# Performance work log

Hardware: AMD Instinct MI355X
Metric: run time of the kernel (lower is better)

Reference implementation:

```python
import jax, jax.numpy as jnp
import numpy as np

N_NODES = 50000
N_EDGES = 1600000
NFEAT, NHID, NCLASS = 512, 128, 40


def setup_inputs() -> dict:
    key = jax.random.key(0)
    ks = jax.random.split(key, 10)
    x = jax.random.normal(ks[0], (N_NODES, NFEAT), dtype=jnp.float32)
    edge_src = jax.random.randint(ks[1], (N_EDGES,), 0, N_NODES, dtype=jnp.int32)
    edge_dst = jax.random.randint(ks[2], (N_EDGES,), 0, N_NODES, dtype=jnp.int32)
    edge_weight = jax.random.uniform(ks[3], (N_EDGES,), dtype=jnp.float32)
    # GraphConvolution params: gc1 (nfeat->nhid), one additional (nhid->nhid), gc2 (nhid->nclass)
    s1 = 1.0 / np.sqrt(NHID)
    s2 = 1.0 / np.sqrt(NCLASS)
    W1 = jax.random.uniform(ks[4], (NFEAT, NHID), minval=-s1, maxval=s1, dtype=jnp.float32)
    b1 = jax.random.uniform(ks[5], (NHID,), minval=-s1, maxval=s1, dtype=jnp.float32)
    Wh = jax.random.uniform(ks[6], (NHID, NHID), minval=-s1, maxval=s1, dtype=jnp.float32)
    bh = jax.random.uniform(ks[7], (NHID,), minval=-s1, maxval=s1, dtype=jnp.float32)
    W2 = jax.random.uniform(ks[8], (NHID, NCLASS), minval=-s2, maxval=s2, dtype=jnp.float32)
    b2 = jax.random.uniform(ks[9], (NCLASS,), minval=-s2, maxval=s2, dtype=jnp.float32)
    return {"x": x, "edge_src": edge_src, "edge_dst": edge_dst, "edge_weight": edge_weight,
            "W1": W1, "b1": b1, "Wh": Wh, "bh": bh, "W2": W2, "b2": b2}


def reference(x, edge_src, edge_dst, edge_weight, W1, b1, Wh, bh, W2, b2):
    def spmm(h):
        # out[i] = sum_j adj[i, j] * h[j]  with adj given as weighted edge list (src=j, dst=i)
        return jax.ops.segment_sum(edge_weight[:, None] * h[edge_src], edge_dst,
                                   num_segments=x.shape[0])

    def gconv(h, W, b):
        return spmm(h @ W) + b  # dense transform then sparse aggregation

    h = jax.nn.relu(gconv(x, W1, b1))       # gc1
    h = jax.nn.relu(gconv(h, Wh, bh))        # additional hidden layer
    h = gconv(h, W2, b2)                     # gc2
    return jax.nn.log_softmax(h, axis=1)
```

## Files before the change

kernel.cpp:

```cpp
#include <hip/hip_runtime.h>
#include <hip/hip_bf16.h>
#include <hip/hip_fp8.h>
#include <math.h>

#define N_NODES 50000
#define N_EDGES 1600000
#define NFEAT 512
#define NHID 128
#define NCLASS 40

#define NBUCKETS 196
#define BUCKET_CAP 16384

typedef __attribute__((ext_vector_type(8))) short bf16x8;
typedef __attribute__((ext_vector_type(4))) float f32x4;
typedef __attribute__((ext_vector_type(2))) float f32x2;

static __device__ __forceinline__ float asfloat_u32(unsigned int u) {
    union { unsigned int u; float f; } c;
    c.u = u;
    return c.f;
}
static __device__ __forceinline__ unsigned int asu32_f(float f) {
    union { float f; unsigned int u; } c;
    c.f = f;
    return c.u;
}
static __device__ __forceinline__ unsigned short f2bf(float f) {
    union { float f; unsigned int u; } c;
    c.f = f;
    unsigned int r = c.u + 0x7FFFu + ((c.u >> 16) & 1u);
    return (unsigned short)(r >> 16);
}

static __device__ __forceinline__ float fp8_to_f32_sw(unsigned int x) {
    float m = asfloat_u32((x & 0x7Fu) << 20) * 0x1p+120f;
    return asfloat_u32(asu32_f(m) | ((x & 0x80u) << 24));
}
static __device__ __forceinline__ void dq4(unsigned int u, float* f) {
#if __has_builtin(__builtin_amdgcn_cvt_pk_f32_fp8)
    f32x2 lo = __builtin_amdgcn_cvt_pk_f32_fp8(u, false);
    f32x2 hi = __builtin_amdgcn_cvt_pk_f32_fp8(u, true);
    f[0] = lo[0]; f[1] = lo[1]; f[2] = hi[0]; f[3] = hi[1];
#else
    f[0] = fp8_to_f32_sw(u & 0xFFu);
    f[1] = fp8_to_f32_sw((u >> 8) & 0xFFu);
    f[2] = fp8_to_f32_sw((u >> 16) & 0xFFu);
    f[3] = fp8_to_f32_sw((u >> 24) & 0xFFu);
#endif
}
static __device__ __forceinline__ unsigned char f2fp8(float f) {
#if __has_builtin(__builtin_amdgcn_cvt_pk_fp8_f32)
    int v = __builtin_amdgcn_cvt_pk_fp8_f32(f, f, 0, false);
    return (unsigned char)(v & 0xFF);
#else
    __hip_fp8_e4m3 h(f);
    return (unsigned char)h.__x;
#endif
}

__global__ __launch_bounds__(256) void prep_kernel(const float* __restrict__ W1,
                                                   unsigned short* __restrict__ Wt1,
                                                   const float* __restrict__ Wh,
                                                   unsigned short* __restrict__ Wth,
                                                   const float* __restrict__ W2,
                                                   unsigned short* __restrict__ Wt2,
                                                   int* __restrict__ bucketCursor) {
    int idx = blockIdx.x * 256 + threadIdx.x;
    if (idx < NFEAT * NHID) {
        int k = idx >> 7;
        int n = idx & 127;
        Wt1[(size_t)n * NFEAT + k] = f2bf(W1[idx]);
    } else if (idx < NFEAT * NHID + NHID * NHID) {
        int j = idx - NFEAT * NHID;
        int k = j >> 7;
        int n = j & 127;
        Wth[(size_t)n * NHID + k] = f2bf(Wh[j]);
    } else if (idx < NFEAT * NHID + NHID * NHID + 64 * NHID) {
        int j = idx - (NFEAT * NHID + NHID * NHID);
        int n = j & 63;
        int k = j >> 6;
        Wt2[(size_t)n * NHID + k] = (n < NCLASS) ? f2bf(W2[(size_t)k * NCLASS + n]) : 0;
    } else {
        int j = idx - (NFEAT * NHID + NHID * NHID + 64 * NHID);
        if (j < NBUCKETS) bucketCursor[j] = j * BUCKET_CAP;
    }
}

#define LDPB 72
#define GEMM_LDS_BYTES (128 * LDPB * 2)

template <bool A_IS_BF16, bool OUT_FP8>
static __device__ __forceinline__ void gemm64_body(const void* __restrict__ Ap,
                                                   const unsigned short* __restrict__ Wt,
                                                   void* __restrict__ Cv,
                                                   const int M, const int K,
                                                   char* smem, int bid) {
    unsigned short* Bs = (unsigned short*)smem;
    const int tid = threadIdx.x;
    const int wave = tid >> 6;
    const int lane = tid & 63;
    const int ln = lane & 15;
    const int quad = lane >> 4;
    const int row0 = bid * 64;

    const int arow = row0 + wave * 16 + ln;
    const bool aOk = arow < M;
    const unsigned short* Abf = (const unsigned short*)Ap + (size_t)arow * K + quad * 8;
    const float* Af = (const float*)Ap + (size_t)arow * K + quad * 8;

    const int bn = tid >> 1;
    const int bk = (tid & 1) * 32;
    const unsigned short* Bg = Wt + (size_t)bn * K + bk;

    f32x4 acc[8];
#pragma unroll
    for (int t = 0; t < 8; ++t) acc[t] = (f32x4){0.f, 0.f, 0.f, 0.f};

    for (int kc = 0; kc < K; kc += 64) {
        bf16x8 qb0 = *(const bf16x8*)(Bg + kc);
        bf16x8 qb1 = *(const bf16x8*)(Bg + kc + 8);
        bf16x8 qb2 = *(const bf16x8*)(Bg + kc + 16);
        bf16x8 qb3 = *(const bf16x8*)(Bg + kc + 24);

        bf16x8 a0, a1;
        if (A_IS_BF16) {
            if (aOk) {
                a0 = *(const bf16x8*)(Abf + kc);
                a1 = *(const bf16x8*)(Abf + kc + 32);
            } else {
#pragma unroll
                for (int j = 0; j < 8; ++j) { a0[j] = 0; a1[j] = 0; }
            }
        } else {
            if (aOk) {
                float4 f0 = *(const float4*)(Af + kc);
                float4 f1 = *(const float4*)(Af + kc + 4);
                float4 f2 = *(const float4*)(Af + kc + 32);
                float4 f3 = *(const float4*)(Af + kc + 36);
                a0[0] = (short)f2bf(f0.x); a0[1] = (short)f2bf(f0.y);
                a0[2] = (short)f2bf(f0.z); a0[3] = (short)f2bf(f0.w);
                a0[4] = (short)f2bf(f1.x); a0[5] = (short)f2bf(f1.y);
                a0[6] = (short)f2bf(f1.z); a0[7] = (short)f2bf(f1.w);
                a1[0] = (short)f2bf(f2.x); a1[1] = (short)f2bf(f2.y);
                a1[2] = (short)f2bf(f2.z); a1[3] = (short)f2bf(f2.w);
                a1[4] = (short)f2bf(f3.x); a1[5] = (short)f2bf(f3.y);
                a1[6] = (short)f2bf(f3.z); a1[7] = (short)f2bf(f3.w);
            } else {
#pragma unroll
                for (int j = 0; j < 8; ++j) { a0[j] = 0; a1[j] = 0; }
            }
        }

        __syncthreads();
        *(bf16x8*)&Bs[bn * LDPB + bk] = qb0;
        *(bf16x8*)&Bs[bn * LDPB + bk + 8] = qb1;
        *(bf16x8*)&Bs[bn * LDPB + bk + 16] = qb2;
        *(bf16x8*)&Bs[bn * LDPB + bk + 24] = qb3;
        __syncthreads();

#pragma unroll
        for (int t = 0; t < 8; ++t) {
            bf16x8 b0 = *(const bf16x8*)&Bs[(t * 16 + ln) * LDPB + quad * 8];
            acc[t] = __builtin_amdgcn_mfma_f32_16x16x32_bf16(a0, b0, acc[t], 0, 0, 0);
        }
#pragma unroll
        for (int t = 0; t < 8; ++t) {
            bf16x8 b1 = *(const bf16x8*)&Bs[(t * 16 + ln) * LDPB + 32 + quad * 8];
            acc[t] = __builtin_amdgcn_mfma_f32_16x16x32_bf16(a1, b1, acc[t], 0, 0, 0);
        }
    }

    if (OUT_FP8) {
        unsigned char* C8 = (unsigned char*)Cv;
#pragma unroll
        for (int t = 0; t < 8; ++t) {
#pragma unroll
            for (int r = 0; r < 4; ++r) {
                int row = row0 + wave * 16 + quad * 4 + r;
                if (row < M) C8[(size_t)row * 128 + t * 16 + ln] = f2fp8(acc[t][r]);
            }
        }
    } else {
        unsigned short* C = (unsigned short*)Cv;
#pragma unroll
        for (int t = 0; t < 8; ++t) {
#pragma unroll
            for (int r = 0; r < 4; ++r) {
                int row = row0 + wave * 16 + quad * 4 + r;
                if (row < M) C[(size_t)row * 128 + t * 16 + ln] = f2bf(acc[t][r]);
            }
        }
    }
}

static __device__ __forceinline__ void bin_body(const int* __restrict__ src,
                                                const int* __restrict__ dst,
                                                const float* __restrict__ w,
                                                int* __restrict__ bucketCursor,
                                                uint2* __restrict__ binned,
                                                int n, char* smem, int bid) {
    int* hist = (int*)smem;
    int* cur = (int*)smem + NBUCKETS;
    const int tid = threadIdx.x;
    const int base = bid * 4096;
    if (tid < NBUCKETS) hist[tid] = 0;
    __syncthreads();
#pragma unroll
    for (int r = 0; r < 16; ++r) {
        int e = base + r * 256 + tid;
        if (e < n) atomicAdd(&hist[dst[e] >> 8], 1);
    }
    __syncthreads();
    if (tid < NBUCKETS && hist[tid] > 0)
        cur[tid] = atomicAdd(&bucketCursor[tid], hist[tid]);
    __syncthreads();
#pragma unroll
    for (int r = 0; r < 16; ++r) {
        int e = base + r * 256 + tid;
        if (e < n) {
            int d = dst[e];
            int pos = atomicAdd(&cur[d >> 8], 1);
            uint2 rec;
            rec.x = (unsigned int)src[e] | ((unsigned int)(d & 255) << 16);
            rec.y = asu32_f(w[e]);
            binned[pos] = rec;
        }
    }
}

#define GEMM1_BLOCKS 782
#define BIN_BLOCKS 391
__global__ __launch_bounds__(256) void fused_gemm1_bin(const float* __restrict__ x,
                                                       const unsigned short* __restrict__ Wt1,
                                                       unsigned char* __restrict__ tb,
                                                       const int* __restrict__ src,
                                                       const int* __restrict__ dst,
                                                       const float* __restrict__ w,
                                                       int* __restrict__ bucketCursor,
                                                       uint2* __restrict__ binned) {
    __shared__ char smem[GEMM_LDS_BYTES];
    if (blockIdx.x < GEMM1_BLOCKS) {
        gemm64_body<false, true>(x, Wt1, tb, N_NODES, NFEAT, smem, blockIdx.x);
    } else {
        bin_body(src, dst, w, bucketCursor, binned, N_EDGES, smem,
                 blockIdx.x - GEMM1_BLOCKS);
    }
}

__global__ __launch_bounds__(256) void gemm64_l2(const unsigned short* __restrict__ A,
                                                 const unsigned short* __restrict__ Wt,
                                                 unsigned char* __restrict__ C) {
    __shared__ char smem[GEMM_LDS_BYTES];
    gemm64_body<true, true>(A, Wt, C, N_NODES, NHID, smem, blockIdx.x);
}

__global__ __launch_bounds__(1024) void build_csr(const uint2* __restrict__ binned,
                                                  const int* __restrict__ bucketCursor,
                                                  unsigned int* __restrict__ pairs,
                                                  int* __restrict__ row_ptr) {
    __shared__ int bs[256];
    __shared__ int hist[256];
    __shared__ int sc[256];
    __shared__ int cur[256];
    const int b = blockIdx.x;
    const int tid = threadIdx.x;

    if (tid < 256) bs[tid] = (tid < NBUCKETS) ? (bucketCursor[tid] - tid * BUCKET_CAP) : 0;
    if (tid < 256) hist[tid] = 0;
    __syncthreads();
    for (int off = 1; off < 256; off <<= 1) {
        int t = 0;
        if (tid < 256 && tid >= off) t = bs[tid - off];
        __syncthreads();
        if (tid < 256) bs[tid] += t;
        __syncthreads();
    }
    const int cnt = bucketCursor[b] - b * BUCKET_CAP;
    const int segStart = bs[b] - cnt;
    if (b == NBUCKETS - 1 && tid == 0) row_ptr[N_NODES] = bs[NBUCKETS - 1];
    const uint2* seg = binned + (size_t)b * BUCKET_CAP;

    for (int i = tid; i < cnt; i += 1024)
        atomicAdd(&hist[seg[i].x >> 16], 1);
    __syncthreads();
    if (tid < 256) {
        int v = hist[tid];
        sc[tid] = v;
    }
    __syncthreads();
    for (int off = 1; off < 256; off <<= 1) {
        int t = 0;
        if (tid < 256 && tid >= off) t = sc[tid - off];
        __syncthreads();
        if (tid < 256) sc[tid] += t;
        __syncthreads();
    }
    if (tid < 256) {
        int excl = sc[tid] - hist[tid];
        int node = b * 256 + tid;
        if (node < N_NODES) row_ptr[node] = segStart + excl;
        cur[tid] = segStart + excl;
    }
    __syncthreads();
    for (int i = tid; i < cnt; i += 1024) {
        uint2 p = seg[i];
        int pos = atomicAdd(&cur[p.x >> 16], 1);
        pairs[pos] = (p.x & 0xFFFFu) | ((unsigned int)f2bf(asfloat_u32(p.y)) << 16);
    }
}

#define LDP2 136
__global__ __launch_bounds__(256) void gemm_n64(const unsigned short* __restrict__ A,
                                                const unsigned short* __restrict__ Wt2,
                                                unsigned short* __restrict__ C, int M) {
    __shared__ unsigned short As[64 * LDP2];
    __shared__ unsigned short Bs[64 * LDP2];
    const int tid = threadIdx.x;
    const int wave = tid >> 6;
    const int lane = tid & 63;
    const int ln = lane & 15;
    const int quad = lane >> 4;
    const int row0 = blockIdx.x * 64;

#pragma unroll
    for (int i = 0; i < 4; ++i) {
        int q = tid + 256 * i;
        int r = q >> 4;
        int c = (q & 15) * 8;
        bf16x8 v;
        if (row0 + r < M) {
            v = *(const bf16x8*)(A + (size_t)(row0 + r) * 128 + c);
        } else {
#pragma unroll
            for (int j = 0; j < 8; ++j) v[j] = 0;
        }
        *(bf16x8*)&As[r * LDP2 + c] = v;
    }
#pragma unroll
    for (int i = 0; i < 4; ++i) {
        int q = tid + 256 * i;
        int r = q >> 4;
        int c = (q & 15) * 8;
        *(bf16x8*)&Bs[r * LDP2 + c] = *(const bf16x8*)(Wt2 + (size_t)r * 128 + c);
    }
    __syncthreads();

    f32x4 acc[4];
#pragma unroll
    for (int t = 0; t < 4; ++t) acc[t] = (f32x4){0.f, 0.f, 0.f, 0.f};

#pragma unroll
    for (int kc = 0; kc < 128; kc += 32) {
        bf16x8 a = *(const bf16x8*)&As[(wave * 16 + ln) * LDP2 + kc + quad * 8];
#pragma unroll
        for (int t = 0; t < 4; ++t) {
            bf16x8 b = *(const bf16x8*)&Bs[(t * 16 + ln) * LDP2 + kc + quad * 8];
            acc[t] = __builtin_amdgcn_mfma_f32_16x16x32_bf16(a, b, acc[t], 0, 0, 0);
        }
    }

#pragma unroll
    for (int t = 0; t < 4; ++t) {
#pragma unroll
        for (int r = 0; r < 4; ++r) {
            int row = row0 + wave * 16 + quad * 4 + r;
            if (row < M) C[(size_t)row * 64 + t * 16 + ln] = f2bf(acc[t][r]);
        }
    }
}

__global__ __launch_bounds__(256) void spmm_bias_relu_fp8(const unsigned char* __restrict__ t,
                                                          const int* __restrict__ row_ptr,
                                                          const unsigned int* __restrict__ pairs,
                                                          const float* __restrict__ bias,
                                                          unsigned short* __restrict__ out) {
    const int node = blockIdx.x * 4 + (threadIdx.x >> 6);
    const int lane = threadIdx.x & 63;
    const int g = lane >> 4;
    const int fl = (lane & 15) * 8;
    const int e0 = row_ptr[node];
    const int e1 = row_ptr[node + 1];
    float acc8[8];
#pragma unroll
    for (int j = 0; j < 8; ++j) acc8[j] = 0.f;

    int e = e0;
    for (; e + 32 <= e1; e += 32) {
        unsigned int p[8];
        uint2 v[8];
#pragma unroll
        for (int i = 0; i < 8; ++i) p[i] = pairs[e + 4 * i + g];
#pragma unroll
        for (int i = 0; i < 8; ++i)
            v[i] = *(const uint2*)(t + (size_t)(p[i] & 0xFFFFu) * 128 + fl);
#pragma unroll
        for (int i = 0; i < 8; ++i) {
            float w = asfloat_u32(p[i] & 0xFFFF0000u);
            float f[8];
            dq4(v[i].x, f);
            dq4(v[i].y, f + 4);
#pragma unroll
            for (int j = 0; j < 8; ++j) acc8[j] += w * f[j];
        }
    }
    for (; e + 4 <= e1; e += 4) {
        unsigned int p = pairs[e + g];
        uint2 v = *(const uint2*)(t + (size_t)(p & 0xFFFFu) * 128 + fl);
        float w = asfloat_u32(p & 0xFFFF0000u);
        float f[8];
        dq4(v.x, f);
        dq4(v.y, f + 4);
#pragma unroll
        for (int j = 0; j < 8; ++j) acc8[j] += w * f[j];
    }
    if (g < e1 - e) {
        unsigned int p = pairs[e + g];
        uint2 v = *(const uint2*)(t + (size_t)(p & 0xFFFFu) * 128 + fl);
        float w = asfloat_u32(p & 0xFFFF0000u);
        float f[8];
        dq4(v.x, f);
        dq4(v.y, f + 4);
#pragma unroll
        for (int j = 0; j < 8; ++j) acc8[j] += w * f[j];
    }
#pragma unroll
    for (int j = 0; j < 8; ++j) {
        acc8[j] += __shfl_xor(acc8[j], 16);
        acc8[j] += __shfl_xor(acc8[j], 32);
    }
    if (g == 0) {
        float4 b0 = *(const float4*)&bias[fl];
        float4 b1 = *(const float4*)&bias[fl + 4];
        acc8[0] = fmaxf(acc8[0] + b0.x, 0.f);
        acc8[1] = fmaxf(acc8[1] + b0.y, 0.f);
        acc8[2] = fmaxf(acc8[2] + b0.z, 0.f);
        acc8[3] = fmaxf(acc8[3] + b0.w, 0.f);
        acc8[4] = fmaxf(acc8[4] + b1.x, 0.f);
        acc8[5] = fmaxf(acc8[5] + b1.y, 0.f);
        acc8[6] = fmaxf(acc8[6] + b1.z, 0.f);
        acc8[7] = fmaxf(acc8[7] + b1.w, 0.f);
        uint4 o;
        o.x = ((unsigned int)f2bf(acc8[0])) | (((unsigned int)f2bf(acc8[1])) << 16);
        o.y = ((unsigned int)f2bf(acc8[2])) | (((unsigned int)f2bf(acc8[3])) << 16);
        o.z = ((unsigned int)f2bf(acc8[4])) | (((unsigned int)f2bf(acc8[5])) << 16);
        o.w = ((unsigned int)f2bf(acc8[6])) | (((unsigned int)f2bf(acc8[7])) << 16);
        *(uint4*)(out + (size_t)node * 128 + fl) = o;
    }
}

__global__ __launch_bounds__(256) void spmm_logsoftmax(const unsigned short* __restrict__ t,
                                                       const int* __restrict__ row_ptr,
                                                       const unsigned int* __restrict__ pairs,
                                                       const float* __restrict__ bias,
                                                       float* __restrict__ out) {
    const int node = blockIdx.x * 4 + (threadIdx.x >> 6);
    const int lane = threadIdx.x & 63;
    const int g = lane >> 4;
    const int fe = (lane & 15) * 4;
    const int e0 = row_ptr[node];
    const int e1 = row_ptr[node + 1];
    float a0 = 0.f, a1 = 0.f, a2 = 0.f, a3 = 0.f;
    int e = e0;
    for (; e + 32 <= e1; e += 32) {
        unsigned int p[8];
        uint2 v[8];
#pragma unroll
        for (int i = 0; i < 8; ++i) p[i] = pairs[e + 4 * i + g];
#pragma unroll
        for (int i = 0; i < 8; ++i)
            v[i] = *(const uint2*)(t + (size_t)(p[i] & 0xFFFFu) * 64 + fe);
#pragma unroll
        for (int i = 0; i < 8; ++i) {
            float w = asfloat_u32(p[i] & 0xFFFF0000u);
            a0 += w * asfloat_u32(v[i].x << 16);
            a1 += w * asfloat_u32(v[i].x & 0xFFFF0000u);
            a2 += w * asfloat_u32(v[i].y << 16);
            a3 += w * asfloat_u32(v[i].y & 0xFFFF0000u);
        }
    }
    for (; e + 4 <= e1; e += 4) {
        unsigned int p = pairs[e + g];
        uint2 v = *(const uint2*)(t + (size_t)(p & 0xFFFFu) * 64 + fe);
        float w = asfloat_u32(p & 0xFFFF0000u);
        a0 += w * asfloat_u32(v.x << 16);
        a1 += w * asfloat_u32(v.x & 0xFFFF0000u);
        a2 += w * asfloat_u32(v.y << 16);
        a3 += w * asfloat_u32(v.y & 0xFFFF0000u);
    }
    if (g < e1 - e) {
        unsigned int p = pairs[e + g];
        uint2 v = *(const uint2*)(t + (size_t)(p & 0xFFFFu) * 64 + fe);
        float w = asfloat_u32(p & 0xFFFF0000u);
        a0 += w * asfloat_u32(v.x << 16);
        a1 += w * asfloat_u32(v.x & 0xFFFF0000u);
        a2 += w * asfloat_u32(v.y << 16);
        a3 += w * asfloat_u32(v.y & 0xFFFF0000u);
    }
    a0 += __shfl_xor(a0, 16); a0 += __shfl_xor(a0, 32);
    a1 += __shfl_xor(a1, 16); a1 += __shfl_xor(a1, 32);
    a2 += __shfl_xor(a2, 16); a2 += __shfl_xor(a2, 32);
    a3 += __shfl_xor(a3, 16); a3 += __shfl_xor(a3, 32);

    const bool valid = (lane & 15) < 10;
    float l0 = -INFINITY, l1 = -INFINITY, l2 = -INFINITY, l3 = -INFINITY;
    if (valid) {
        float4 b = *(const float4*)&bias[fe];
        l0 = a0 + b.x; l1 = a1 + b.y; l2 = a2 + b.z; l3 = a3 + b.w;
    }
    float m = fmaxf(fmaxf(l0, l1), fmaxf(l2, l3));
#pragma unroll
    for (int off = 8; off; off >>= 1) m = fmaxf(m, __shfl_xor(m, off));
    float s = valid ? (__expf(l0 - m) + __expf(l1 - m) + __expf(l2 - m) + __expf(l3 - m)) : 0.f;
#pragma unroll
    for (int off = 8; off; off >>= 1) s += __shfl_xor(s, off);
    if (valid && g == 0) {
        float ls = __logf(s);
        float4 o;
        o.x = l0 - m - ls; o.y = l1 - m - ls; o.z = l2 - m - ls; o.w = l3 - m - ls;
        *(float4*)&out[(size_t)node * NCLASS + fe] = o;
    }
}


extern "C" void kernel_launch(void* const* d_in, const int* in_sizes, int n_in,
                              void* d_out, int out_size, void* d_ws, size_t ws_size,
                              hipStream_t stream) {
    const float* x = (const float*)d_in[0];
    const int* edge_src = (const int*)d_in[1];
    const int* edge_dst = (const int*)d_in[2];
    const float* edge_weight = (const float*)d_in[3];
    const float* W1 = (const float*)d_in[4];
    const float* b1 = (const float*)d_in[5];
    const float* Wh = (const float*)d_in[6];
    const float* bh = (const float*)d_in[7];
    const float* W2 = (const float*)d_in[8];
    const float* b2 = (const float*)d_in[9];
    float* out = (float*)d_out;

    size_t off = 0;
    auto carve = [&](size_t bytes) {
        void* p = (char*)d_ws + off;
        off += (bytes + 511) & ~(size_t)511;
        return p;
    };
    unsigned char* tb = (unsigned char*)carve((size_t)N_NODES * 128);
    unsigned short* hb = (unsigned short*)carve((size_t)N_NODES * 128 * 2);
    unsigned short* t3 = (unsigned short*)carve((size_t)N_NODES * 64 * 2);
    unsigned short* Wt1 = (unsigned short*)carve((size_t)NFEAT * NHID * 2);
    unsigned short* Wth = (unsigned short*)carve((size_t)NHID * NHID * 2);
    unsigned short* Wt2 = (unsigned short*)carve((size_t)64 * NHID * 2);
    int* row_ptr = (int*)carve((size_t)(N_NODES + 4) * 4);
    int* bucketCursor = (int*)carve((size_t)NBUCKETS * 4);
    uint2* binned = (uint2*)carve((size_t)NBUCKETS * BUCKET_CAP * 8);
    unsigned int* pairs = (unsigned int*)carve((size_t)N_EDGES * 4);
    (void)ws_size; (void)n_in; (void)in_sizes; (void)out_size;

    const int prepBlocks =
        (NFEAT * NHID + NHID * NHID + 64 * NHID + NBUCKETS + 255) / 256;
    const int spmmBlocks = N_NODES / 4;
    const int gemmBlocks = (N_NODES + 63) / 64;

    prep_kernel<<<prepBlocks, 256, 0, stream>>>(W1, Wt1, Wh, Wth, W2, Wt2, bucketCursor);

    fused_gemm1_bin<<<GEMM1_BLOCKS + BIN_BLOCKS, 256, 0, stream>>>(
        x, Wt1, tb, edge_src, edge_dst, edge_weight, bucketCursor, binned);

    build_csr<<<NBUCKETS, 1024, 0, stream>>>(binned, bucketCursor, pairs, row_ptr);

    spmm_bias_relu_fp8<<<spmmBlocks, 256, 0, stream>>>(tb, row_ptr, pairs, b1, hb);

    gemm64_l2<<<gemmBlocks, 256, 0, stream>>>(hb, Wth, tb);
    spmm_bias_relu_fp8<<<spmmBlocks, 256, 0, stream>>>(tb, row_ptr, pairs, bh, hb);

    gemm_n64<<<gemmBlocks, 256, 0, stream>>>(hb, Wt2, t3, N_NODES);
    spmm_logsoftmax<<<spmmBlocks, 256, 0, stream>>>(t3, row_ptr, pairs, b2, out);
}
```

Measured before the change: 360.4 us.

## Split fused gemm1/bin kernel into separate kernels with finer-grained binning

Replaces the single launch that ran GEMM1 blocks and edge-binning blocks side by side with two launches: a standalone binning kernel followed by the GEMM1 kernel. The binning kernel now handles 1024 edges per block over 1563 blocks instead of 4096 over 391, and keeps its small histogram in its own shared arrays rather than the large GEMM LDS allocation. The aim is more parallelism and higher occupancy for binning, at the cost of losing the overlap between binning and GEMM1, adding a kernel launch, and issuing roughly four times as many global cursor atomics.

Result: slower. 395.8 us (+9.8%).

```diff
diff --git a/kernel.cpp b/kernel.cpp
--- a/kernel.cpp
+++ b/kernel.cpp
@@ -194,31 +194,45 @@
     }
 }
 
-static __device__ __forceinline__ void bin_body(const int* __restrict__ src,
-                                                const int* __restrict__ dst,
-                                                const float* __restrict__ w,
-                                                int* __restrict__ bucketCursor,
-                                                uint2* __restrict__ binned,
-                                                int n, char* smem, int bid) {
-    int* hist = (int*)smem;
-    int* cur = (int*)smem + NBUCKETS;
+__global__ __launch_bounds__(256) void gemm1_kernel(const float* __restrict__ x,
+                                                    const unsigned short* __restrict__ Wt1,
+                                                    unsigned char* __restrict__ tb) {
+    __shared__ char smem[GEMM_LDS_BYTES];
+    gemm64_body<false, true>(x, Wt1, tb, N_NODES, NFEAT, smem, blockIdx.x);
+}
+
+__global__ __launch_bounds__(256) void gemm64_l2(const unsigned short* __restrict__ A,
+                                                 const unsigned short* __restrict__ Wt,
+                                                 unsigned char* __restrict__ C) {
+    __shared__ char smem[GEMM_LDS_BYTES];
+    gemm64_body<true, true>(A, Wt, C, N_NODES, NHID, smem, blockIdx.x);
+}
+
+#define BIN_BLOCKS 1563
+__global__ __launch_bounds__(256) void bin_kernel(const int* __restrict__ src,
+                                                  const int* __restrict__ dst,
+                                                  const float* __restrict__ w,
+                                                  int* __restrict__ bucketCursor,
+                                                  uint2* __restrict__ binned) {
+    __shared__ int hist[NBUCKETS];
+    __shared__ int cur[NBUCKETS];
     const int tid = threadIdx.x;
-    const int base = bid * 4096;
+    const int base = blockIdx.x * 1024;
     if (tid < NBUCKETS) hist[tid] = 0;
     __syncthreads();
 #pragma unroll
-    for (int r = 0; r < 16; ++r) {
+    for (int r = 0; r < 4; ++r) {
         int e = base + r * 256 + tid;
-        if (e < n) atomicAdd(&hist[dst[e] >> 8], 1);
+        if (e < N_EDGES) atomicAdd(&hist[dst[e] >> 8], 1);
     }
     __syncthreads();
     if (tid < NBUCKETS && hist[tid] > 0)
         cur[tid] = atomicAdd(&bucketCursor[tid], hist[tid]);
     __syncthreads();
 #pragma unroll
-    for (int r = 0; r < 16; ++r) {
+    for (int r = 0; r < 4; ++r) {
         int e = base + r * 256 + tid;
-        if (e < n) {
+        if (e < N_EDGES) {
             int d = dst[e];
             int pos = atomicAdd(&cur[d >> 8], 1);
             uint2 rec;
@@ -227,32 +241,6 @@
             binned[pos] = rec;
         }
     }
-}
-
-#define GEMM1_BLOCKS 782
-#define BIN_BLOCKS 391
-__global__ __launch_bounds__(256) void fused_gemm1_bin(const float* __restrict__ x,
-                                                       const unsigned short* __restrict__ Wt1,
-                                                       unsigned char* __restrict__ tb,
-                                                       const int* __restrict__ src,
-                                                       const int* __restrict__ dst,
-                                                       const float* __restrict__ w,
-                                                       int* __restrict__ bucketCursor,
-                                                       uint2* __restrict__ binned) {
-    __shared__ char smem[GEMM_LDS_BYTES];
-    if (blockIdx.x < GEMM1_BLOCKS) {
-        gemm64_body<false, true>(x, Wt1, tb, N_NODES, NFEAT, smem, blockIdx.x);
-    } else {
-        bin_body(src, dst, w, bucketCursor, binned, N_EDGES, smem,
-                 blockIdx.x - GEMM1_BLOCKS);
-    }
-}
-
-__global__ __launch_bounds__(256) void gemm64_l2(const unsigned short* __restrict__ A,
-                                                 const unsigned short* __restrict__ Wt,
-                                                 unsigned char* __restrict__ C) {
-    __shared__ char smem[GEMM_LDS_BYTES];
-    gemm64_body<true, true>(A, Wt, C, N_NODES, NHID, smem, blockIdx.x);
 }
 
 __global__ __launch_bounds__(1024) void build_csr(const uint2* __restrict__ binned,
@@ -563,8 +551,9 @@
 
     prep_kernel<<<prepBlocks, 256, 0, stream>>>(W1, Wt1, Wh, Wth, W2, Wt2, bucketCursor);
 
-    fused_gemm1_bin<<<GEMM1_BLOCKS + BIN_BLOCKS, 256, 0, stream>>>(
-        x, Wt1, tb, edge_src, edge_dst, edge_weight, bucketCursor, binned);
+    bin_kernel<<<BIN_BLOCKS, 256, 0, stream>>>(edge_src, edge_dst, edge_weight,
+                                               bucketCursor, binned);
+    gemm1_kernel<<<gemmBlocks, 256, 0, stream>>>(x, Wt1, tb);
 
     build_csr<<<NBUCKETS, 1024, 0, stream>>>(binned, bucketCursor, pairs, row_ptr);
 
```

## Store layer-3 transform in fp8 and specialize layer-2 GEMM with register-resident A

Applied to the files above, without the earlier changes.

The final-layer transformed features t3 are now written as fp8 instead of bf16, halving the bytes gathered per edge in the log-softmax SpMM, which dequantizes four values per 32-bit load. Separately, the hidden-layer GEMM is rewritten as a dedicated kernel that loads A rows directly into registers and stages only the weight matrix in LDS, with K fully unrolled. The fp8 change trades accuracy in the output logits for lower gather bandwidth. The GEMM rewrite removes the generic tiled body for this K=128 case.

Measured after the change: 355.9 us, median of 2. Within noise of the previous version (-1.3%).

```diff
diff --git a/kernel.cpp b/kernel.cpp
--- a/kernel.cpp
+++ b/kernel.cpp
@@ -248,11 +248,74 @@
     }
 }
 
+#define LDP2 136
 __global__ __launch_bounds__(256) void gemm64_l2(const unsigned short* __restrict__ A,
                                                  const unsigned short* __restrict__ Wt,
                                                  unsigned char* __restrict__ C) {
-    __shared__ char smem[GEMM_LDS_BYTES];
-    gemm64_body<true, true>(A, Wt, C, N_NODES, NHID, smem, blockIdx.x);
+    __shared__ unsigned short Bs[128 * LDP2];
+    const int tid = threadIdx.x;
+    const int wave = tid >> 6;
+    const int lane = tid & 63;
+    const int ln = lane & 15;
+    const int quad = lane >> 4;
+    const int row0 = blockIdx.x * 64;
+    const int arow = row0 + wave * 16 + ln;
+    const bool aOk = arow < N_NODES;
+    const unsigned short* Abf = A + (size_t)arow * 128 + quad * 8;
+
+    bf16x8 a0, a1, a2, a3;
+    if (aOk) {
+        a0 = *(const bf16x8*)(Abf);
+        a1 = *(const bf16x8*)(Abf + 32);
+        a2 = *(const bf16x8*)(Abf + 64);
+        a3 = *(const bf16x8*)(Abf + 96);
+    } else {
+#pragma unroll
+        for (int j = 0; j < 8; ++j) { a0[j] = 0; a1[j] = 0; a2[j] = 0; a3[j] = 0; }
+    }
+
+#pragma unroll
+    for (int i = 0; i < 8; ++i) {
+        int q = tid + 256 * i;
+        int r = q >> 4;
+        int c = (q & 15) * 8;
+        *(bf16x8*)&Bs[r * LDP2 + c] = *(const bf16x8*)(Wt + (size_t)r * 128 + c);
+    }
+    __syncthreads();
+
+    f32x4 acc[8];
+#pragma unroll
+    for (int t = 0; t < 8; ++t) acc[t] = (f32x4){0.f, 0.f, 0.f, 0.f};
+
+#pragma unroll
+    for (int t = 0; t < 8; ++t) {
+        bf16x8 b = *(const bf16x8*)&Bs[(t * 16 + ln) * LDP2 + quad * 8];
+        acc[t] = __builtin_amdgcn_mfma_f32_16x16x32_bf16(a0, b, acc[t], 0, 0, 0);
+    }
+#pragma unroll
+    for (int t = 0; t < 8; ++t) {
+        bf16x8 b = *(const bf16x8*)&Bs[(t * 16 + ln) * LDP2 + 32 + quad * 8];
+        acc[t] = __builtin_amdgcn_mfma_f32_16x16x32_bf16(a1, b, acc[t], 0, 0, 0);
+    }
+#pragma unroll
+    for (int t = 0; t < 8; ++t) {
+        bf16x8 b = *(const bf16x8*)&Bs[(t * 16 + ln) * LDP2 + 64 + quad * 8];
+        acc[t] = __builtin_amdgcn_mfma_f32_16x16x32_bf16(a2, b, acc[t], 0, 0, 0);
+    }
+#pragma unroll
+    for (int t = 0; t < 8; ++t) {
+        bf16x8 b = *(const bf16x8*)&Bs[(t * 16 + ln) * LDP2 + 96 + quad * 8];
+        acc[t] = __builtin_amdgcn_mfma_f32_16x16x32_bf16(a3, b, acc[t], 0, 0, 0);
+    }
+
+#pragma unroll
+    for (int t = 0; t < 8; ++t) {
+#pragma unroll
+        for (int r = 0; r < 4; ++r) {
+            int row = row0 + wave * 16 + quad * 4 + r;
+            if (row < N_NODES) C[(size_t)row * 128 + t * 16 + ln] = f2fp8(acc[t][r]);
+        }
+    }
 }
 
 __global__ __launch_bounds__(1024) void build_csr(const uint2* __restrict__ binned,
@@ -310,12 +373,11 @@
     }
 }
 
-#define LDP2 136
 __global__ __launch_bounds__(256) void gemm_n64(const unsigned short* __restrict__ A,
                                                 const unsigned short* __restrict__ Wt2,
-                                                unsigned short* __restrict__ C, int M) {
+                                                unsigned char* __restrict__ C, int M) {
     __shared__ unsigned short As[64 * LDP2];
-    __shared__ unsigned short Bs[64 * LDP2];
+    __shared__ unsigned short Bs2[64 * LDP2];
     const int tid = threadIdx.x;
     const int wave = tid >> 6;
     const int lane = tid & 63;
@@ -342,7 +404,7 @@
         int q = tid + 256 * i;
         int r = q >> 4;
         int c = (q & 15) * 8;
-        *(bf16x8*)&Bs[r * LDP2 + c] = *(const bf16x8*)(Wt2 + (size_t)r * 128 + c);
+        *(bf16x8*)&Bs2[r * LDP2 + c] = *(const bf16x8*)(Wt2 + (size_t)r * 128 + c);
     }
     __syncthreads();
 
@@ -355,7 +417,7 @@
         bf16x8 a = *(const bf16x8*)&As[(wave * 16 + ln) * LDP2 + kc + quad * 8];
 #pragma unroll
         for (int t = 0; t < 4; ++t) {
-            bf16x8 b = *(const bf16x8*)&Bs[(t * 16 + ln) * LDP2 + kc + quad * 8];
+            bf16x8 b = *(const bf16x8*)&Bs2[(t * 16 + ln) * LDP2 + kc + quad * 8];
             acc[t] = __builtin_amdgcn_mfma_f32_16x16x32_bf16(a, b, acc[t], 0, 0, 0);
         }
     }
@@ -365,7 +427,7 @@
 #pragma unroll
         for (int r = 0; r < 4; ++r) {
             int row = row0 + wave * 16 + quad * 4 + r;
-            if (row < M) C[(size_t)row * 64 + t * 16 + ln] = f2bf(acc[t][r]);
+            if (row < M) C[(size_t)row * 64 + t * 16 + ln] = f2fp8(acc[t][r]);
         }
     }
 }
@@ -449,7 +511,7 @@
     }
 }
 
-__global__ __launch_bounds__(256) void spmm_logsoftmax(const unsigned short* __restrict__ t,
+__global__ __launch_bounds__(256) void spmm_logsoftmax(const unsigned char* __restrict__ t,
                                                        const int* __restrict__ row_ptr,
                                                        const unsigned int* __restrict__ pairs,
                                                        const float* __restrict__ bias,
@@ -464,38 +526,38 @@
     int e = e0;
     for (; e + 32 <= e1; e += 32) {
         unsigned int p[8];
-        uint2 v[8];
+        unsigned int v[8];
 #pragma unroll
         for (int i = 0; i < 8; ++i) p[i] = pairs[e + 4 * i + g];
 #pragma unroll
         for (int i = 0; i < 8; ++i)
-            v[i] = *(const uint2*)(t + (size_t)(p[i] & 0xFFFFu) * 64 + fe);
+            v[i] = *(const unsigned int*)(t + (size_t)(p[i] & 0xFFFFu) * 64 + fe);
 #pragma unroll
         for (int i = 0; i < 8; ++i) {
             float w = asfloat_u32(p[i] & 0xFFFF0000u);
-            a0 += w * asfloat_u32(v[i].x << 16);
-            a1 += w * asfloat_u32(v[i].x & 0xFFFF0000u);
-            a2 += w * asfloat_u32(v[i].y << 16);
-            a3 += w * asfloat_u32(v[i].y & 0xFFFF0000u);
+            float f[4];
+            dq4(v[i], f);
+            a0 += w * f[0];
+            a1 += w * f[1];
+            a2 += w * f[2];
+            a3 += w * f[3];
         }
     }
     for (; e + 4 <= e1; e += 4) {
         unsigned int p = pairs[e + g];
-        uint2 v = *(const uint2*)(t + (size_t)(p & 0xFFFFu) * 64 + fe);
+        unsigned int v = *(const unsigned int*)(t + (size_t)(p & 0xFFFFu) * 64 + fe);
         float w = asfloat_u32(p & 0xFFFF0000u);
-        a0 += w * asfloat_u32(v.x << 16);
-        a1 += w * asfloat_u32(v.x & 0xFFFF0000u);
-        a2 += w * asfloat_u32(v.y << 16);
-        a3 += w * asfloat_u32(v.y & 0xFFFF0000u);
+        float f[4];
+        dq4(v, f);
+        a0 += w * f[0]; a1 += w * f[1]; a2 += w * f[2]; a3 += w * f[3];
     }
     if (g < e1 - e) {
         unsigned int p = pairs[e + g];
-        uint2 v = *(const uint2*)(t + (size_t)(p & 0xFFFFu) * 64 + fe);
+        unsigned int v = *(const unsigned int*)(t + (size_t)(p & 0xFFFFu) * 64 + fe);
         float w = asfloat_u32(p & 0xFFFF0000u);
-        a0 += w * asfloat_u32(v.x << 16);
-        a1 += w * asfloat_u32(v.x & 0xFFFF0000u);
-        a2 += w * asfloat_u32(v.y << 16);
-        a3 += w * asfloat_u32(v.y & 0xFFFF0000u);
+        float f[4];
+        dq4(v, f);
+        a0 += w * f[0]; a1 += w * f[1]; a2 += w * f[2]; a3 += w * f[3];
     }
     a0 += __shfl_xor(a0, 16); a0 += __shfl_xor(a0, 32);
     a1 += __shfl_xor(a1, 16); a1 += __shfl_xor(a1, 32);
@@ -546,7 +608,7 @@
     };
     unsigned char* tb = (unsigned char*)carve((size_t)N_NODES * 128);
     unsigned short* hb = (unsigned short*)carve((size_t)N_NODES * 128 * 2);
-    unsigned short* t3 = (unsigned short*)carve((size_t)N_NODES * 64 * 2);
+    unsigned char* t3 = (unsigned char*)carve((size_t)N_NODES * 64);
     unsigned short* Wt1 = (unsigned short*)carve((size_t)NFEAT * NHID * 2);
     unsigned short* Wth = (unsigned short*)carve((size_t)NHID * NHID * 2);
     unsigned short* Wt2 = (unsigned short*)carve((size_t)64 * NHID * 2);
```
